# Kernel optimization log

Hardware: AMD Instinct MI355X
Metric: run time of the kernel (lower is better)

The kernel has to match this reference:

```python
import jax, jax.numpy as jnp
import numpy as np

N = 100000   # nodes
E = 1600000  # edges (avg degree 16)
F_IN, F_HID, F_OUT = 128, 128, 64


def _glorot_like(key, shape, fan_in):
    s = 1.0 / np.sqrt(fan_in)
    return jax.random.uniform(key, shape, jnp.float32, -s, s)


def setup_inputs():
    key = jax.random.key(0)
    ks = jax.random.split(key, 10)
    x = jax.random.normal(ks[0], (N, F_IN), jnp.float32)
    edge_index = jax.random.randint(ks[1], (2, E), 0, N, dtype=jnp.int64)
    # layer 0: GCNConv(128->128) + Linear(128->128)
    W0 = _glorot_like(ks[2], (F_IN, F_HID), F_IN)
    b0 = jnp.zeros((F_HID,), jnp.float32)
    Wl0 = _glorot_like(ks[3], (F_IN, F_HID), F_IN)
    bl0 = _glorot_like(ks[4], (F_HID,), F_IN)
    # layer 1: GCNConv(128->64) + Linear(128->64)
    W1 = _glorot_like(ks[5], (F_HID, F_OUT), F_HID)
    b1 = jnp.zeros((F_OUT,), jnp.float32)
    Wl1 = _glorot_like(ks[6], (F_HID, F_OUT), F_HID)
    bl1 = _glorot_like(ks[7], (F_OUT,), F_HID)
    return {"x": x, "edge_index": edge_index, "W0": W0, "b0": b0,
            "Wl0": Wl0, "bl0": bl0, "W1": W1, "b1": b1,
            "Wl1": Wl1, "bl1": bl1}


def _gcn_conv(x, W, b, src, dst, n):
    # PyG GCNConv: out = D^{-1/2} (A + I) D^{-1/2} (x W) + b
    h = x @ W                                      # [n, f_out]
    deg = jnp.ones((n,), x.dtype).at[dst].add(1.0)  # in-degree incl. self-loop
    dinv = jax.lax.rsqrt(deg)                      # [n]
    coef = dinv[src] * dinv[dst]                   # [E] edge norm
    agg = jax.ops.segment_sum(h[src] * coef[:, None], dst, num_segments=n)
    agg = agg + h * (dinv * dinv)[:, None]         # self-loop contribution
    return agg + b


def reference(x, edge_index, W0, b0, Wl0, bl0, W1, b1, Wl1, bl1):
    n = x.shape[0]
    src, dst = edge_index[0], edge_index[1]
    # layer 0 (inductive): conv(x) + lin(x), relu; dropout is identity in eval
    h = jax.nn.relu(_gcn_conv(x, W0, b0, src, dst, n) + x @ Wl0 + bl0)
    # output layer
    return _gcn_conv(h, W1, b1, src, dst, n) + h @ Wl1 + bl1
```

## Files before the change

### kernel.cpp

```cpp
#include <hip/hip_runtime.h>
#include <hip/hip_bf16.h>

#define NN 100000
#define EE 1600000
#define FF 128
#define FO 64

#define NR 256
#define RSZ 391
#define BCAP 8192
#define SE 5000
#define SBLK 320
#define GBLK0 782

typedef unsigned int u32;
typedef unsigned short u16;
typedef short s16x8 __attribute__((ext_vector_type(8)));
typedef float f32x4 __attribute__((ext_vector_type(4)));

__device__ __forceinline__ float bf_lo(u32 v) { return __uint_as_float(v << 16); }
__device__ __forceinline__ float bf_hi(u32 v) { return __uint_as_float(v & 0xffff0000u); }
__device__ __forceinline__ u16 f2bf(float f) {
    __hip_bfloat16 h = __float2bfloat16(f);
    return *(u16*)&h;
}
__device__ __forceinline__ u32 pk2(float a, float b) {
    return (u32)f2bf(a) | ((u32)f2bf(b) << 16);
}

__device__ __forceinline__ int ld_dst(const u32* w, int e, int f) {
    return f ? (int)w[2u * (u32)(EE + e)] : (int)w[(u32)(EE + e)];
}
__device__ __forceinline__ int ld_src(const u32* w, int e, int f) {
    return f ? (int)w[2u * (u32)e] : (int)w[(u32)e];
}

__device__ __forceinline__ int wave_iscan(int v, int lane) {
#pragma unroll
    for (int off = 1; off < 64; off <<= 1) {
        int t = __shfl_up(v, off);
        if (lane >= off) v += t;
    }
    return v;
}

__global__ __launch_bounds__(256) void k_prep(
    const float* __restrict__ W0, const float* __restrict__ Wl0,
    const float* __restrict__ b0, const float* __restrict__ bl0,
    const float* __restrict__ W1, const float* __restrict__ Wl1,
    const float* __restrict__ b1, const float* __restrict__ bl1,
    uint4* __restrict__ pb0, uint4* __restrict__ pb1,
    float* __restrict__ bb0, float* __restrict__ bb1) {
    const int t = threadIdx.x;
    if (blockIdx.x == 0 && t < FF) bb0[t] = b0[t] + bl0[t];
    if (blockIdx.x == 1 && t < FO) bb1[t] = b1[t] + bl1[t];
    int slot = blockIdx.x * 256 + t;
    if (slot < 4096) {
        int lane = slot & 63, nt = (slot >> 6) & 15, kb = slot >> 10;
        int c = 16 * nt + (lane & 15);
        int k0 = 32 * kb + 8 * (lane >> 4);
        u32 u[4];
#pragma unroll
        for (int p = 0; p < 4; ++p) {
            int ka = k0 + 2 * p, kb2 = k0 + 2 * p + 1;
            float v0 = (c < FF) ? W0[(size_t)ka * FF + c] : Wl0[(size_t)ka * FF + c - FF];
            float v1 = (c < FF) ? W0[(size_t)kb2 * FF + c] : Wl0[(size_t)kb2 * FF + c - FF];
            u[p] = pk2(v0, v1);
        }
        pb0[slot] = make_uint4(u[0], u[1], u[2], u[3]);
    } else if (slot < 6144) {
        int s = slot - 4096;
        int lane = s & 63, nt = (s >> 6) & 7, kb = s >> 9;
        int c = 16 * nt + (lane & 15);
        int q = 4 * kb + (lane >> 4);
        u32 u[4];
#pragma unroll
        for (int p = 0; p < 4; ++p) {
            int ra = 16 * (2 * p) + q;
            int rb = 16 * (2 * p + 1) + q;
            float v0 = (c < FO) ? W1[(size_t)ra * FO + c] : Wl1[(size_t)ra * FO + c - FO];
            float v1 = (c < FO) ? W1[(size_t)rb * FO + c] : Wl1[(size_t)rb * FO + c - FO];
            u[p] = pk2(v0, v1);
        }
        pb1[s] = make_uint4(u[0], u[1], u[2], u[3]);
    }
}

union SMem {
    struct {
        u16 inv[SE]; unsigned char rng[SE];
        int hist[NR], excl[NR], cur[NR], gbase[NR]; int wsum[8]; u32 fl;
    } sc;
    uint4 aLDS[128 * 16];
};

__device__ void role_gemm0(int bid, const float* __restrict__ x,
                           const uint4* __restrict__ pb0,
                           const float* __restrict__ bb0,
                           uint2* __restrict__ h0f8, uint4* __restrict__ linb4,
                           SMem& sm) {
    const int tid = threadIdx.x;
    const int n0 = bid * 128;
    {
        int r = tid >> 2, q = tid & 3;
        int node = n0 + r;
        uint4 ov[4];
        if (node < NN) {
            const float* src = &x[(size_t)node * FF + 32 * q];
#pragma unroll
            for (int i = 0; i < 4; ++i) {
                float4 f0 = *(const float4*)(src + 8 * i);
                float4 f1 = *(const float4*)(src + 8 * i + 4);
                ov[i] = make_uint4(pk2(f0.x, f0.y), pk2(f0.z, f0.w),
                                   pk2(f1.x, f1.y), pk2(f1.z, f1.w));
            }
        } else {
#pragma unroll
            for (int i = 0; i < 4; ++i) ov[i] = make_uint4(0, 0, 0, 0);
        }
#pragma unroll
        for (int i = 0; i < 4; ++i) {
            int chunk = 4 * q + i;
            sm.aLDS[r * 16 + (chunk ^ (r & 7))] = ov[i];
        }
    }
    __syncthreads();
    const int w = tid >> 6, l = tid & 63;
    const int lrow = l & 15, lhi = l >> 4;
    const int arow = 16 * w + lrow;
    f32x4 acc[16] = {};
#pragma unroll
    for (int kb = 0; kb < 4; ++kb) {
        int chunk = 4 * kb + lhi;
        uint4 av = sm.aLDS[arow * 16 + (chunk ^ (arow & 7))];
        s16x8 a = __builtin_bit_cast(s16x8, av);
#pragma unroll
        for (int nt = 0; nt < 16; ++nt) {
            uint4 bv = pb0[(kb * 16 + nt) * 64 + l];
            s16x8 b = __builtin_bit_cast(s16x8, bv);
            acc[nt] = __builtin_amdgcn_mfma_f32_16x16x32_bf16(a, b, acc[nt], 0, 0, 0);
        }
    }
#pragma unroll
    for (int j = 0; j < 4; ++j) {
        int node = n0 + 16 * w + 4 * lhi + j;
        u32 w0 = (u32)__builtin_amdgcn_cvt_pk_fp8_f32(acc[0][j], acc[1][j], 0, false);
        w0 = (u32)__builtin_amdgcn_cvt_pk_fp8_f32(acc[2][j], acc[3][j], (int)w0, true);
        u32 w1 = (u32)__builtin_amdgcn_cvt_pk_fp8_f32(acc[4][j], acc[5][j], 0, false);
        w1 = (u32)__builtin_amdgcn_cvt_pk_fp8_f32(acc[6][j], acc[7][j], (int)w1, true);
        h0f8[(size_t)node * 16 + lrow] = make_uint2(w0, w1);
        if (node >= NN) continue;
        uint4 lb;
        lb.x = pk2(acc[8][j] + bb0[lrow],       acc[9][j] + bb0[16 + lrow]);
        lb.y = pk2(acc[10][j] + bb0[32 + lrow], acc[11][j] + bb0[48 + lrow]);
        lb.z = pk2(acc[12][j] + bb0[64 + lrow], acc[13][j] + bb0[80 + lrow]);
        lb.w = pk2(acc[14][j] + bb0[96 + lrow], acc[15][j] + bb0[112 + lrow]);
        linb4[(size_t)node * 16 + lrow] = lb;
    }
}

__device__ void role_scatter(int sbid, const void* __restrict__ ei,
                             int* __restrict__ gCur, uint2* __restrict__ pairB,
                             SMem& sm) {
    const int tid = threadIdx.x;
    const int lane = tid & 63, wid = tid >> 6;
    const u32* w = (const u32*)ei;
    const int e0 = sbid * SE;
    if (tid == 0) sm.sc.fl = 0;
    if (tid < NR) { sm.sc.hist[tid] = 0; sm.sc.cur[tid] = 0; }
    __syncthreads();
    {
        u32 acc = 0;
#pragma unroll
        for (int r = 0; r < 4; ++r) acc |= w[2u * (u32)(e0 + tid + 512 * r) + 1];
        if (acc) atomicOr(&sm.sc.fl, 1u);
    }
    __syncthreads();
    const int f = (sm.sc.fl == 0) ? 1 : 0;
    for (int i = tid; i < SE; i += 512) {
        int dv = ld_dst(w, e0 + i, f);
        u32 r = (u32)dv / RSZ;
        sm.sc.rng[i] = (unsigned char)r;
        atomicAdd(&sm.sc.hist[r], 1);
    }
    __syncthreads();
    int v = (tid < NR) ? sm.sc.hist[tid] : 0;
    v = wave_iscan(v, lane);
    if (lane == 63) sm.sc.wsum[wid] = v;
    __syncthreads();
    if (tid < NR) {
        int add = 0;
#pragma unroll
        for (int k = 0; k < 3; ++k)
            if (k < wid) add += sm.sc.wsum[k];
        int incl = v + add;
        sm.sc.excl[tid] = incl - sm.sc.hist[tid];
        int r2 = (tid + sbid) & (NR - 1);
        sm.sc.gbase[r2] = atomicAdd(&gCur[r2], sm.sc.hist[r2]);
    }
    __syncthreads();
    for (int i = tid; i < SE; i += 512) {
        int r = sm.sc.rng[i];
        int p = atomicAdd(&sm.sc.cur[r], 1);
        sm.sc.inv[sm.sc.excl[r] + p] = (u16)i;
    }
    __syncthreads();
    for (int s = tid; s < SE; s += 512) {
        int i = sm.sc.inv[s];
        int r = sm.sc.rng[i];
        int dv = ld_dst(w, e0 + i, f);
        int sv = ld_src(w, e0 + i, f);
        int g = sm.sc.gbase[r] + (s - sm.sc.excl[r]);
        if (g < BCAP)
            pairB[(size_t)r * BCAP + g] = make_uint2((u32)dv, (u32)sv);
    }
}

__global__ __launch_bounds__(512) void k_mega(
    const float* __restrict__ x, const void* __restrict__ ei,
    int* __restrict__ gCur, uint2* __restrict__ pairB,
    const uint4* __restrict__ pb0, const float* __restrict__ bb0,
    uint2* __restrict__ h0f8, uint4* __restrict__ linb4) {
    __shared__ SMem sm;
    const int bid = blockIdx.x;
    if (bid < SBLK) {
        role_scatter(bid, ei, gCur, pairB, sm);
    } else {
        role_gemm0(bid - SBLK, x, pb0, bb0, h0f8, linb4, sm);
    }
}

__global__ __launch_bounds__(512) void k_fillrange(const uint2* __restrict__ pairB,
                                                   const int* __restrict__ gCur,
                                                   int* __restrict__ rp,
                                                   float* __restrict__ dinv,
                                                   int* __restrict__ col) {
    __shared__ int colbuf[BCAP];
    __shared__ int hist[RSZ], scn[RSZ], cur[RSZ];
    __shared__ int rb[NR];
    __shared__ int wsum[8];
    const int r = blockIdx.x;
    const int tid = threadIdx.x;
    const int lane = tid & 63, wid = tid >> 6;
    {
        int v = (tid < NR) ? gCur[tid] : 0;
        v = wave_iscan(v, lane);
        if (lane == 63) wsum[wid] = v;
        __syncthreads();
        if (tid < NR) {
            int add = 0;
#pragma unroll
            for (int k = 0; k < 3; ++k)
                if (k < wid) add += wsum[k];
            rb[tid] = v + add;
        }
        __syncthreads();
    }
    const int base = (r == 0) ? 0 : rb[r - 1];
    if (r == 0 && tid == 0) rp[NN] = rb[NR - 1];
    const int n = min(gCur[r], BCAP);
    const uint2* pb = &pairB[(size_t)r * BCAP];
    const int v0 = r * RSZ;
    for (int i = tid; i < RSZ; i += 512) { hist[i] = 0; cur[i] = 0; }
    __syncthreads();
    for (int j = tid; j < n; j += 512) atomicAdd(&hist[(int)pb[j].x - v0], 1);
    __syncthreads();
    {
        int v = (tid < RSZ) ? hist[tid] : 0;
        v = wave_iscan(v, lane);
        if (lane == 63) wsum[wid] = v;
        __syncthreads();
        int add = 0;
#pragma unroll
        for (int k = 0; k < 7; ++k)
            if (k < wid) add += wsum[k];
        if (tid < RSZ) scn[tid] = v + add;
    }
    if (tid < RSZ) {
        int v = v0 + tid;
        if (v < NN) {
            rp[v] = base + scn[tid] - hist[tid];
            dinv[v] = rsqrtf((float)hist[tid] + 1.0f);
        }
    }
    __syncthreads();
    for (int j = tid; j < n; j += 512) {
        uint2 pr = pb[j];
        int li = (int)pr.x - v0;
        int p = atomicAdd(&cur[li], 1);
        colbuf[scn[li] - hist[li] + p] = (int)pr.y;
    }
    __syncthreads();
    for (int j = tid; j < n; j += 512) col[base + j] = colbuf[j];
}

__global__ __launch_bounds__(256) void k_agg0(
    const int* __restrict__ rp, const int* __restrict__ col,
    const float* __restrict__ dinv, const uint2* __restrict__ h0f8,
    const uint4* __restrict__ linb4, uint4* __restrict__ hb) {
    const int i = blockIdx.x * 4 + (threadIdx.x >> 6);
    if (i >= NN) return;
    const int l = threadIdx.x & 63;
    const int q = l >> 4;
    const int c = l & 15;
    const int e0 = rp[i];
    const int cnt = rp[i + 1] - e0;
    const int cntv = cnt + 1;
    int j0;
    float dvL;
    if (l < cnt) {
        j0 = col[e0 + l];
        dvL = dinv[j0];
    } else if (l == cnt) {
        j0 = i;
        dvL = dinv[i];
    } else {
        j0 = NN;
        dvL = 0.f;
    }
    int offL = j0 << 7;
    const u32 oc = 8u * (u32)c;
    const char* hb8 = (const char*)h0f8;
    float a0 = 0.f, a1 = 0.f, a2 = 0.f, a3 = 0.f;
    float a4 = 0.f, a5 = 0.f, a6 = 0.f, a7 = 0.f;
#define ACC_FP8(vv, dd)                                                      \
    {                                                                        \
        auto d0 = __builtin_amdgcn_cvt_pk_f32_fp8((vv).x, false);            \
        auto d1 = __builtin_amdgcn_cvt_pk_f32_fp8((vv).x, true);             \
        auto d2 = __builtin_amdgcn_cvt_pk_f32_fp8((vv).y, false);            \
        auto d3 = __builtin_amdgcn_cvt_pk_f32_fp8((vv).y, true);             \
        a0 = fmaf(dd, d0[0], a0); a1 = fmaf(dd, d0[1], a1);                  \
        a2 = fmaf(dd, d1[0], a2); a3 = fmaf(dd, d1[1], a3);                  \
        a4 = fmaf(dd, d2[0], a4); a5 = fmaf(dd, d2[1], a5);                  \
        a6 = fmaf(dd, d3[0], a6); a7 = fmaf(dd, d3[1], a7);                  \
    }
    const int T = (min(cntv, 64) + 3) >> 2;
    int k = 0;
    for (; k + 4 <= T; k += 4) {
        int s = q + 4 * k;
        int oA = __shfl(offL, s);
        int oB = __shfl(offL, s + 4);
        int oC = __shfl(offL, s + 8);
        int oD = __shfl(offL, s + 12);
        float dA = __shfl(dvL, s);
        float dB = __shfl(dvL, s + 4);
        float dC = __shfl(dvL, s + 8);
        float dD = __shfl(dvL, s + 12);
        uint2 vA = *(const uint2*)(hb8 + ((u32)oA + oc));
        uint2 vB = *(const uint2*)(hb8 + ((u32)oB + oc));
        uint2 vC = *(const uint2*)(hb8 + ((u32)oC + oc));
        uint2 vD = *(const uint2*)(hb8 + ((u32)oD + oc));
        ACC_FP8(vA, dA);
        ACC_FP8(vB, dB);
        ACC_FP8(vC, dC);
        ACC_FP8(vD, dD);
    }
    for (; k < T; ++k) {
        int s = q + 4 * k;
        int o = __shfl(offL, s);
        float d = __shfl(dvL, s);
        uint2 v = *(const uint2*)(hb8 + ((u32)o + oc));
        ACC_FP8(v, d);
    }
    for (int e = 64 + q; e < cntv; e += 4) {
        int j = (e < cnt) ? col[e0 + e] : i;
        float d = dinv[j];
        uint2 v = *(const uint2*)(hb8 + ((u32)(j << 7) + oc));
        ACC_FP8(v, d);
    }
#undef ACC_FP8
#pragma unroll
    for (int off = 16; off < 64; off <<= 1) {
        a0 += __shfl_xor(a0, off);
        a1 += __shfl_xor(a1, off);
        a2 += __shfl_xor(a2, off);
        a3 += __shfl_xor(a3, off);
        a4 += __shfl_xor(a4, off);
        a5 += __shfl_xor(a5, off);
        a6 += __shfl_xor(a6, off);
        a7 += __shfl_xor(a7, off);
    }
    if (q == 0) {
        float di = dinv[i];
        uint4 lb = linb4[(size_t)i * 16 + c];
        uint4 ov;
        ov.x = pk2(fmaxf(fmaf(di, a0, bf_lo(lb.x)), 0.f),
                   fmaxf(fmaf(di, a1, bf_hi(lb.x)), 0.f));
        ov.y = pk2(fmaxf(fmaf(di, a2, bf_lo(lb.y)), 0.f),
                   fmaxf(fmaf(di, a3, bf_hi(lb.y)), 0.f));
        ov.z = pk2(fmaxf(fmaf(di, a4, bf_lo(lb.z)), 0.f),
                   fmaxf(fmaf(di, a5, bf_hi(lb.z)), 0.f));
        ov.w = pk2(fmaxf(fmaf(di, a6, bf_lo(lb.w)), 0.f),
                   fmaxf(fmaf(di, a7, bf_hi(lb.w)), 0.f));
        hb[(size_t)i * 16 + c] = ov;
    }
}

__global__ __launch_bounds__(256) void k_gemm1(
    const u16* __restrict__ h, const uint4* __restrict__ pb1,
    const float* __restrict__ bb1, const float* __restrict__ dinv,
    u16* __restrict__ h1s, float* __restrict__ out) {
    __shared__ uint4 aLDS[64 * 16];
    const int tid = threadIdx.x;
    const int n0 = blockIdx.x * 64;
    {
        int r = tid >> 2, q = tid & 3;
        int node = n0 + r;
        uint4 ov[4];
        if (node < NN) {
            const uint4* src = (const uint4*)&h[(size_t)node * FF + 32 * q];
#pragma unroll
            for (int i = 0; i < 4; ++i) ov[i] = src[i];
        } else {
#pragma unroll
            for (int i = 0; i < 4; ++i) ov[i] = make_uint4(0, 0, 0, 0);
        }
#pragma unroll
        for (int i = 0; i < 4; ++i) {
            int chunk = 4 * q + i;
            aLDS[r * 16 + (chunk ^ (r & 7))] = ov[i];
        }
    }
    __syncthreads();
    const int w = tid >> 6, l = tid & 63;
    const int lrow = l & 15, lhi = l >> 4;
    const int arow = 16 * w + lrow;
    f32x4 acc[8] = {};
#pragma unroll
    for (int kb = 0; kb < 4; ++kb) {
        int chunk = 4 * kb + lhi;
        uint4 av = aLDS[arow * 16 + (chunk ^ (arow & 7))];
        s16x8 a = __builtin_bit_cast(s16x8, av);
#pragma unroll
        for (int nt = 0; nt < 8; ++nt) {
            uint4 bv = pb1[(kb * 8 + nt) * 64 + l];
            s16x8 b = __builtin_bit_cast(s16x8, bv);
            acc[nt] = __builtin_amdgcn_mfma_f32_16x16x32_bf16(a, b, acc[nt], 0, 0, 0);
        }
    }
#pragma unroll
    for (int j = 0; j < 4; ++j) {
        int node = n0 + 16 * w + 4 * lhi + j;
        if (node >= NN) {
#pragma unroll
            for (int nt = 0; nt < 4; ++nt)
                h1s[(size_t)node * FO + 16 * nt + lrow] = 0;
            continue;
        }
        float di = dinv[node], d2 = di * di;
#pragma unroll
        for (int nt = 0; nt < 4; ++nt) {
            int c = 16 * nt + lrow;
            float hv = acc[nt][j];
            float lv = acc[nt + 4][j];
            h1s[(size_t)node * FO + c] = f2bf(di * hv);
            out[(size_t)node * FO + c] = fmaf(hv, d2, lv + bb1[c]);
        }
    }
}

__global__ __launch_bounds__(256) void k_agg1(
    const int* __restrict__ rp, const int* __restrict__ col,
    const float* __restrict__ dinv, const uint4* __restrict__ h1s,
    float* __restrict__ out) {
    const int i = blockIdx.x * 4 + (threadIdx.x >> 6);
    if (i >= NN) return;
    const int l = threadIdx.x & 63;
    const int g = l >> 3;
    const int c = l & 7;
    const int e0 = rp[i];
    const int cnt = rp[i + 1] - e0;
    int j0 = (l < cnt) ? col[e0 + l] : NN;
    int offL = j0 << 7;
    const u32 oc = 16u * (u32)c;
    const char* hs8 = (const char*)h1s;
    float a0 = 0.f, a1 = 0.f, a2 = 0.f, a3 = 0.f;
    float a4 = 0.f, a5 = 0.f, a6 = 0.f, a7 = 0.f;
    const int T = (min(cnt, 64) + 7) >> 3;
    int k = 0;
    for (; k + 2 <= T; k += 2) {
        int s = g + 8 * k;
        int oA = __shfl(offL, s);
        int oB = __shfl(offL, s + 8);
        uint4 vA = *(const uint4*)(hs8 + ((u32)oA + oc));
        uint4 vB = *(const uint4*)(hs8 + ((u32)oB + oc));
        a0 += bf_lo(vA.x) + bf_lo(vB.x);
        a1 += bf_hi(vA.x) + bf_hi(vB.x);
        a2 += bf_lo(vA.y) + bf_lo(vB.y);
        a3 += bf_hi(vA.y) + bf_hi(vB.y);
        a4 += bf_lo(vA.z) + bf_lo(vB.z);
        a5 += bf_hi(vA.z) + bf_hi(vB.z);
        a6 += bf_lo(vA.w) + bf_lo(vB.w);
        a7 += bf_hi(vA.w) + bf_hi(vB.w);
    }
    for (; k < T; ++k) {
        int s = g + 8 * k;
        int o = __shfl(offL, s);
        uint4 v = *(const uint4*)(hs8 + ((u32)o + oc));
        a0 += bf_lo(v.x); a1 += bf_hi(v.x); a2 += bf_lo(v.y); a3 += bf_hi(v.y);
        a4 += bf_lo(v.z); a5 += bf_hi(v.z); a6 += bf_lo(v.w); a7 += bf_hi(v.w);
    }
    for (int e = 64 + g; e < cnt; e += 8) {
        int j = col[e0 + e];
        uint4 v = *(const uint4*)(hs8 + ((u32)(j << 7) + oc));
        a0 += bf_lo(v.x); a1 += bf_hi(v.x); a2 += bf_lo(v.y); a3 += bf_hi(v.y);
        a4 += bf_lo(v.z); a5 += bf_hi(v.z); a6 += bf_lo(v.w); a7 += bf_hi(v.w);
    }
#pragma unroll
    for (int off = 8; off < 64; off <<= 1) {
        a0 += __shfl_xor(a0, off);
        a1 += __shfl_xor(a1, off);
        a2 += __shfl_xor(a2, off);
        a3 += __shfl_xor(a3, off);
        a4 += __shfl_xor(a4, off);
        a5 += __shfl_xor(a5, off);
        a6 += __shfl_xor(a6, off);
        a7 += __shfl_xor(a7, off);
    }
    if (g == 0) {
        float di = dinv[i];
        size_t o = (size_t)i * FO + 8 * c;
        float4 c0 = *(const float4*)&out[o];
        float4 c1 = *(const float4*)&out[o + 4];
        c0.x = fmaf(di, a0, c0.x);
        c0.y = fmaf(di, a1, c0.y);
        c0.z = fmaf(di, a2, c0.z);
        c0.w = fmaf(di, a3, c0.w);
        c1.x = fmaf(di, a4, c1.x);
        c1.y = fmaf(di, a5, c1.y);
        c1.z = fmaf(di, a6, c1.z);
        c1.w = fmaf(di, a7, c1.w);
        *(float4*)&out[o] = c0;
        *(float4*)&out[o + 4] = c1;
    }
}

extern "C" void kernel_launch(void* const* d_in, const int* in_sizes, int n_in,
                              void* d_out, int out_size, void* d_ws, size_t ws_size,
                              hipStream_t stream) {
    const float* x   = (const float*)d_in[0];
    const void*  ei  = d_in[1];
    const float* W0  = (const float*)d_in[2];
    const float* b0  = (const float*)d_in[3];
    const float* Wl0 = (const float*)d_in[4];
    const float* bl0 = (const float*)d_in[5];
    const float* W1  = (const float*)d_in[6];
    const float* b1  = (const float*)d_in[7];
    const float* Wl1 = (const float*)d_in[8];
    const float* bl1 = (const float*)d_in[9];
    float* out = (float*)d_out;

    char* p = (char*)d_ws;
    auto alloc = [&](size_t bytes) -> void* {
        void* r = (void*)p;
        p += (bytes + 255) & ~(size_t)255;
        return r;
    };
    int*   gCur   = (int*)alloc(NR * 4);
    int*   rp     = (int*)alloc((size_t)(NN + 1) * 4);
    int*   col    = (int*)alloc((size_t)EE * 4);
    uint2* pairB  = (uint2*)alloc((size_t)NR * BCAP * 8);
    float* dinv   = (float*)alloc((size_t)NN * 4);
    uint4* pb0    = (uint4*)alloc(4096 * 16);
    uint4* pb1    = (uint4*)alloc(2048 * 16);
    float* bb0    = (float*)alloc(FF * 4);
    float* bb1    = (float*)alloc(FO * 4);
    uint2* h0f8   = (uint2*)alloc((size_t)(NN + 128) * FF);
    uint4* linb4  = (uint4*)alloc((size_t)NN * FF * 2);
    u16*   h1s    = (u16*)alloc((size_t)(NN + 64) * FO * 2);
    u16*   hb     = (u16*)alloc((size_t)NN * FF * 2);

    hipMemsetAsync(gCur, 0, NR * 4, stream);
    k_prep<<<24, 256, 0, stream>>>(W0, Wl0, b0, bl0, W1, Wl1, b1, bl1,
                                   pb0, pb1, bb0, bb1);
    k_mega<<<GBLK0 + SBLK, 512, 0, stream>>>(x, ei, gCur, pairB, pb0, bb0,
                                             h0f8, linb4);
    k_fillrange<<<NR, 512, 0, stream>>>(pairB, gCur, rp, dinv, col);
    k_agg0<<<(NN + 3) / 4, 256, 0, stream>>>(rp, col, dinv, h0f8, linb4,
                                             (uint4*)hb);
    k_gemm1<<<(NN + 63) / 64, 256, 0, stream>>>(hb, pb1, bb1, dinv, h1s, out);
    k_agg1<<<(NN + 3) / 4, 256, 0, stream>>>(rp, col, dinv, (const uint4*)h1s, out);
}
```

Baseline: 174.3 us.

## Process four nodes per wave in aggregation and simplify scatter/fillrange staging

Both aggregation kernels now assign four consecutive nodes to each wavefront, prefetching all four row ranges and neighbor indices up front so their loads overlap. The grid shrinks accordingly. The scatter pass drops its local sort-by-range staging and writes pairs directly using per-range atomic cursors. Fillrange writes col entries straight to global memory instead of staging them in shared memory. These cut launch overhead, shared-memory work and barriers, at the cost of less coalesced global writes and more registers per thread.

```diff
diff --git a/kernel.cpp b/kernel.cpp
--- a/kernel.cpp
+++ b/kernel.cpp
@@ -12,6 +12,8 @@
 #define SE 5000
 #define SBLK 320
 #define GBLK0 782
+#define NPW 4
+#define AGG_GRID 6250
 
 typedef unsigned int u32;
 typedef unsigned short u16;
@@ -88,8 +90,7 @@
 
 union SMem {
     struct {
-        u16 inv[SE]; unsigned char rng[SE];
-        int hist[NR], excl[NR], cur[NR], gbase[NR]; int wsum[8]; u32 fl;
+        int hist[NR], cur[NR], gbase[NR]; u32 fl;
     } sc;
     uint4 aLDS[128 * 16];
 };
@@ -163,7 +164,6 @@
                              int* __restrict__ gCur, uint2* __restrict__ pairB,
                              SMem& sm) {
     const int tid = threadIdx.x;
-    const int lane = tid & 63, wid = tid >> 6;
     const u32* w = (const u32*)ei;
     const int e0 = sbid * SE;
     if (tid == 0) sm.sc.fl = 0;
@@ -179,38 +179,20 @@
     const int f = (sm.sc.fl == 0) ? 1 : 0;
     for (int i = tid; i < SE; i += 512) {
         int dv = ld_dst(w, e0 + i, f);
-        u32 r = (u32)dv / RSZ;
-        sm.sc.rng[i] = (unsigned char)r;
-        atomicAdd(&sm.sc.hist[r], 1);
-    }
-    __syncthreads();
-    int v = (tid < NR) ? sm.sc.hist[tid] : 0;
-    v = wave_iscan(v, lane);
-    if (lane == 63) sm.sc.wsum[wid] = v;
+        atomicAdd(&sm.sc.hist[(u32)dv / RSZ], 1);
+    }
     __syncthreads();
     if (tid < NR) {
-        int add = 0;
-#pragma unroll
-        for (int k = 0; k < 3; ++k)
-            if (k < wid) add += sm.sc.wsum[k];
-        int incl = v + add;
-        sm.sc.excl[tid] = incl - sm.sc.hist[tid];
         int r2 = (tid + sbid) & (NR - 1);
         sm.sc.gbase[r2] = atomicAdd(&gCur[r2], sm.sc.hist[r2]);
     }
     __syncthreads();
     for (int i = tid; i < SE; i += 512) {
-        int r = sm.sc.rng[i];
-        int p = atomicAdd(&sm.sc.cur[r], 1);
-        sm.sc.inv[sm.sc.excl[r] + p] = (u16)i;
-    }
-    __syncthreads();
-    for (int s = tid; s < SE; s += 512) {
-        int i = sm.sc.inv[s];
-        int r = sm.sc.rng[i];
         int dv = ld_dst(w, e0 + i, f);
         int sv = ld_src(w, e0 + i, f);
-        int g = sm.sc.gbase[r] + (s - sm.sc.excl[r]);
+        u32 r = (u32)dv / RSZ;
+        int p = atomicAdd(&sm.sc.cur[r], 1);
+        int g = sm.sc.gbase[r] + p;
         if (g < BCAP)
             pairB[(size_t)r * BCAP + g] = make_uint2((u32)dv, (u32)sv);
     }
@@ -235,7 +217,6 @@
                                                    int* __restrict__ rp,
                                                    float* __restrict__ dinv,
                                                    int* __restrict__ col) {
-    __shared__ int colbuf[BCAP];
     __shared__ int hist[RSZ], scn[RSZ], cur[RSZ];
     __shared__ int rb[NR];
     __shared__ int wsum[8];
@@ -288,41 +269,38 @@
         uint2 pr = pb[j];
         int li = (int)pr.x - v0;
         int p = atomicAdd(&cur[li], 1);
-        colbuf[scn[li] - hist[li] + p] = (int)pr.y;
-    }
-    __syncthreads();
-    for (int j = tid; j < n; j += 512) col[base + j] = colbuf[j];
+        col[base + scn[li] - hist[li] + p] = (int)pr.y;
+    }
 }
 
 __global__ __launch_bounds__(256) void k_agg0(
     const int* __restrict__ rp, const int* __restrict__ col,
     const float* __restrict__ dinv, const uint2* __restrict__ h0f8,
     const uint4* __restrict__ linb4, uint4* __restrict__ hb) {
-    const int i = blockIdx.x * 4 + (threadIdx.x >> 6);
-    if (i >= NN) return;
+    const int wv = blockIdx.x * 4 + (threadIdx.x >> 6);
+    const int i0 = wv * NPW;
+    if (i0 >= NN) return;
     const int l = threadIdx.x & 63;
     const int q = l >> 4;
     const int c = l & 15;
-    const int e0 = rp[i];
-    const int cnt = rp[i + 1] - e0;
-    const int cntv = cnt + 1;
-    int j0;
-    float dvL;
-    if (l < cnt) {
-        j0 = col[e0 + l];
-        dvL = dinv[j0];
-    } else if (l == cnt) {
-        j0 = i;
-        dvL = dinv[i];
-    } else {
-        j0 = NN;
-        dvL = 0.f;
-    }
-    int offL = j0 << 7;
+    int rpv = (l <= NPW) ? rp[i0 + l] : 0;
+    int rpk[NPW + 1];
+#pragma unroll
+    for (int k = 0; k <= NPW; ++k) rpk[k] = __shfl(rpv, k);
+    int offL[NPW];
+    float dvL[NPW];
+#pragma unroll
+    for (int k = 0; k < NPW; ++k) {
+        int cntk = rpk[k + 1] - rpk[k];
+        int jj;
+        if (l < cntk) jj = col[rpk[k] + l];
+        else if (l == cntk) jj = i0 + k;
+        else jj = NN;
+        dvL[k] = (jj < NN) ? dinv[jj] : 0.f;
+        offL[k] = jj << 7;
+    }
     const u32 oc = 8u * (u32)c;
     const char* hb8 = (const char*)h0f8;
-    float a0 = 0.f, a1 = 0.f, a2 = 0.f, a3 = 0.f;
-    float a4 = 0.f, a5 = 0.f, a6 = 0.f, a7 = 0.f;
 #define ACC_FP8(vv, dd)                                                      \
     {                                                                        \
         auto d0 = __builtin_amdgcn_cvt_pk_f32_fp8((vv).x, false);            \
@@ -334,66 +312,75 @@
         a4 = fmaf(dd, d2[0], a4); a5 = fmaf(dd, d2[1], a5);                  \
         a6 = fmaf(dd, d3[0], a6); a7 = fmaf(dd, d3[1], a7);                  \
     }
-    const int T = (min(cntv, 64) + 3) >> 2;
-    int k = 0;
-    for (; k + 4 <= T; k += 4) {
-        int s = q + 4 * k;
-        int oA = __shfl(offL, s);
-        int oB = __shfl(offL, s + 4);
-        int oC = __shfl(offL, s + 8);
-        int oD = __shfl(offL, s + 12);
-        float dA = __shfl(dvL, s);
-        float dB = __shfl(dvL, s + 4);
-        float dC = __shfl(dvL, s + 8);
-        float dD = __shfl(dvL, s + 12);
-        uint2 vA = *(const uint2*)(hb8 + ((u32)oA + oc));
-        uint2 vB = *(const uint2*)(hb8 + ((u32)oB + oc));
-        uint2 vC = *(const uint2*)(hb8 + ((u32)oC + oc));
-        uint2 vD = *(const uint2*)(hb8 + ((u32)oD + oc));
-        ACC_FP8(vA, dA);
-        ACC_FP8(vB, dB);
-        ACC_FP8(vC, dC);
-        ACC_FP8(vD, dD);
-    }
-    for (; k < T; ++k) {
-        int s = q + 4 * k;
-        int o = __shfl(offL, s);
-        float d = __shfl(dvL, s);
-        uint2 v = *(const uint2*)(hb8 + ((u32)o + oc));
-        ACC_FP8(v, d);
-    }
-    for (int e = 64 + q; e < cntv; e += 4) {
-        int j = (e < cnt) ? col[e0 + e] : i;
-        float d = dinv[j];
-        uint2 v = *(const uint2*)(hb8 + ((u32)(j << 7) + oc));
-        ACC_FP8(v, d);
+#pragma unroll
+    for (int k = 0; k < NPW; ++k) {
+        const int i = i0 + k;
+        const int cnt = rpk[k + 1] - rpk[k];
+        const int cntv = cnt + 1;
+        float a0 = 0.f, a1 = 0.f, a2 = 0.f, a3 = 0.f;
+        float a4 = 0.f, a5 = 0.f, a6 = 0.f, a7 = 0.f;
+        const int T = (min(cntv, 64) + 3) >> 2;
+        int t = 0;
+        for (; t + 4 <= T; t += 4) {
+            int s = q + 4 * t;
+            int oA = __shfl(offL[k], s);
+            int oB = __shfl(offL[k], s + 4);
+            int oC = __shfl(offL[k], s + 8);
+            int oD = __shfl(offL[k], s + 12);
+            float dA = __shfl(dvL[k], s);
+            float dB = __shfl(dvL[k], s + 4);
+            float dC = __shfl(dvL[k], s + 8);
+            float dD = __shfl(dvL[k], s + 12);
+            uint2 vA = *(const uint2*)(hb8 + ((u32)oA + oc));
+            uint2 vB = *(const uint2*)(hb8 + ((u32)oB + oc));
+            uint2 vC = *(const uint2*)(hb8 + ((u32)oC + oc));
+            uint2 vD = *(const uint2*)(hb8 + ((u32)oD + oc));
+            ACC_FP8(vA, dA);
+            ACC_FP8(vB, dB);
+            ACC_FP8(vC, dC);
+            ACC_FP8(vD, dD);
+        }
+        for (; t < T; ++t) {
+            int s = q + 4 * t;
+            int o = __shfl(offL[k], s);
+            float d = __shfl(dvL[k], s);
+            uint2 v = *(const uint2*)(hb8 + ((u32)o + oc));
+            ACC_FP8(v, d);
+        }
+        for (int e = 64 + q; e < cntv; e += 4) {
+            int j = (e < cnt) ? col[rpk[k] + e] : i;
+            float d = dinv[j];
+            uint2 v = *(const uint2*)(hb8 + ((u32)(j << 7) + oc));
+            ACC_FP8(v, d);
+        }
+#pragma unroll
+        for (int off = 16; off < 64; off <<= 1) {
+            a0 += __shfl_xor(a0, off);
+            a1 += __shfl_xor(a1, off);
+            a2 += __shfl_xor(a2, off);
+            a3 += __shfl_xor(a3, off);
+            a4 += __shfl_xor(a4, off);
+            a5 += __shfl_xor(a5, off);
+            a6 += __shfl_xor(a6, off);
+            a7 += __shfl_xor(a7, off);
+        }
+        float di = __shfl(dvL[k], min(cnt, 63));
+        if (cnt > 63) di = dinv[i];
+        if (q == 0) {
+            uint4 lb = linb4[(size_t)i * 16 + c];
+            uint4 ov;
+            ov.x = pk2(fmaxf(fmaf(di, a0, bf_lo(lb.x)), 0.f),
+                       fmaxf(fmaf(di, a1, bf_hi(lb.x)), 0.f));
+            ov.y = pk2(fmaxf(fmaf(di, a2, bf_lo(lb.y)), 0.f),
+                       fmaxf(fmaf(di, a3, bf_hi(lb.y)), 0.f));
+            ov.z = pk2(fmaxf(fmaf(di, a4, bf_lo(lb.z)), 0.f),
+                       fmaxf(fmaf(di, a5, bf_hi(lb.z)), 0.f));
+            ov.w = pk2(fmaxf(fmaf(di, a6, bf_lo(lb.w)), 0.f),
+                       fmaxf(fmaf(di, a7, bf_hi(lb.w)), 0.f));
+            hb[(size_t)i * 16 + c] = ov;
+        }
     }
 #undef ACC_FP8
-#pragma unroll
-    for (int off = 16; off < 64; off <<= 1) {
-        a0 += __shfl_xor(a0, off);
-        a1 += __shfl_xor(a1, off);
-        a2 += __shfl_xor(a2, off);
-        a3 += __shfl_xor(a3, off);
-        a4 += __shfl_xor(a4, off);
-        a5 += __shfl_xor(a5, off);
-        a6 += __shfl_xor(a6, off);
-        a7 += __shfl_xor(a7, off);
-    }
-    if (q == 0) {
-        float di = dinv[i];
-        uint4 lb = linb4[(size_t)i * 16 + c];
-        uint4 ov;
-        ov.x = pk2(fmaxf(fmaf(di, a0, bf_lo(lb.x)), 0.f),
-                   fmaxf(fmaf(di, a1, bf_hi(lb.x)), 0.f));
-        ov.y = pk2(fmaxf(fmaf(di, a2, bf_lo(lb.y)), 0.f),
-                   fmaxf(fmaf(di, a3, bf_hi(lb.y)), 0.f));
-        ov.z = pk2(fmaxf(fmaf(di, a4, bf_lo(lb.z)), 0.f),
-                   fmaxf(fmaf(di, a5, bf_hi(lb.z)), 0.f));
-        ov.w = pk2(fmaxf(fmaf(di, a6, bf_lo(lb.w)), 0.f),
-                   fmaxf(fmaf(di, a7, bf_hi(lb.w)), 0.f));
-        hb[(size_t)i * 16 + c] = ov;
-    }
 }
 
 __global__ __launch_bounds__(256) void k_gemm1(
@@ -463,75 +450,88 @@
     const int* __restrict__ rp, const int* __restrict__ col,
     const float* __restrict__ dinv, const uint4* __restrict__ h1s,
     float* __restrict__ out) {
-    const int i = blockIdx.x * 4 + (threadIdx.x >> 6);
-    if (i >= NN) return;
+    const int wv = blockIdx.x * 4 + (threadIdx.x >> 6);
+    const int i0 = wv * NPW;
+    if (i0 >= NN) return;
     const int l = threadIdx.x & 63;
     const int g = l >> 3;
     const int c = l & 7;
-    const int e0 = rp[i];
-    const int cnt = rp[i + 1] - e0;
-    int j0 = (l < cnt) ? col[e0 + l] : NN;
-    int offL = j0 << 7;
+    int rpv = (l <= NPW) ? rp[i0 + l] : 0;
+    int rpk[NPW + 1];
+#pragma unroll
+    for (int k = 0; k <= NPW; ++k) rpk[k] = __shfl(rpv, k);
+    int offL[NPW];
+#pragma unroll
+    for (int k = 0; k < NPW; ++k) {
+        int cntk = rpk[k + 1] - rpk[k];
+        int jj = (l < cntk) ? col[rpk[k] + l] : NN;
+        offL[k] = jj << 7;
+    }
     const u32 oc = 16u * (u32)c;
     const char* hs8 = (const char*)h1s;
-    float a0 = 0.f, a1 = 0.f, a2 = 0.f, a3 = 0.f;
-    float a4 = 0.f, a5 = 0.f, a6 = 0.f, a7 = 0.f;
-    const int T = (min(cnt, 64) + 7) >> 3;
-    int k = 0;
-    for (; k + 2 <= T; k += 2) {
-        int s = g + 8 * k;
-        int oA = __shfl(offL, s);
-        int oB = __shfl(offL, s + 8);
-        uint4 vA = *(const uint4*)(hs8 + ((u32)oA + oc));
-        uint4 vB = *(const uint4*)(hs8 + ((u32)oB + oc));
-        a0 += bf_lo(vA.x) + bf_lo(vB.x);
-        a1 += bf_hi(vA.x) + bf_hi(vB.x);
-        a2 += bf_lo(vA.y) + bf_lo(vB.y);
-        a3 += bf_hi(vA.y) + bf_hi(vB.y);
-        a4 += bf_lo(vA.z) + bf_lo(vB.z);
-        a5 += bf_hi(vA.z) + bf_hi(vB.z);
-        a6 += bf_lo(vA.w) + bf_lo(vB.w);
-        a7 += bf_hi(vA.w) + bf_hi(vB.w);
-    }
-    for (; k < T; ++k) {
-        int s = g + 8 * k;
-        int o = __shfl(offL, s);
-        uint4 v = *(const uint4*)(hs8 + ((u32)o + oc));
-        a0 += bf_lo(v.x); a1 += bf_hi(v.x); a2 += bf_lo(v.y); a3 += bf_hi(v.y);
-        a4 += bf_lo(v.z); a5 += bf_hi(v.z); a6 += bf_lo(v.w); a7 += bf_hi(v.w);
-    }
-    for (int e = 64 + g; e < cnt; e += 8) {
-        int j = col[e0 + e];
-        uint4 v = *(const uint4*)(hs8 + ((u32)(j << 7) + oc));
-        a0 += bf_lo(v.x); a1 += bf_hi(v.x); a2 += bf_lo(v.y); a3 += bf_hi(v.y);
-        a4 += bf_lo(v.z); a5 += bf_hi(v.z); a6 += bf_lo(v.w); a7 += bf_hi(v.w);
-    }
-#pragma unroll
-    for (int off = 8; off < 64; off <<= 1) {
-        a0 += __shfl_xor(a0, off);
-        a1 += __shfl_xor(a1, off);
-        a2 += __shfl_xor(a2, off);
-        a3 += __shfl_xor(a3, off);
-        a4 += __shfl_xor(a4, off);
-        a5 += __shfl_xor(a5, off);
-        a6 += __shfl_xor(a6, off);
-        a7 += __shfl_xor(a7, off);
-    }
-    if (g == 0) {
-        float di = dinv[i];
-        size_t o = (size_t)i * FO + 8 * c;
-        float4 c0 = *(const float4*)&out[o];
-        float4 c1 = *(const float4*)&out[o + 4];
-        c0.x = fmaf(di, a0, c0.x);
-        c0.y = fmaf(di, a1, c0.y);
-        c0.z = fmaf(di, a2, c0.z);
-        c0.w = fmaf(di, a3, c0.w);
-        c1.x = fmaf(di, a4, c1.x);
-        c1.y = fmaf(di, a5, c1.y);
-        c1.z = fmaf(di, a6, c1.z);
-        c1.w = fmaf(di, a7, c1.w);
-        *(float4*)&out[o] = c0;
-        *(float4*)&out[o + 4] = c1;
+#pragma unroll
+    for (int k = 0; k < NPW; ++k) {
+        const int i = i0 + k;
+        const int cnt = rpk[k + 1] - rpk[k];
+        float a0 = 0.f, a1 = 0.f, a2 = 0.f, a3 = 0.f;
+        float a4 = 0.f, a5 = 0.f, a6 = 0.f, a7 = 0.f;
+        const int T = (min(cnt, 64) + 7) >> 3;
+        int t = 0;
+        for (; t + 2 <= T; t += 2) {
+            int s = g + 8 * t;
+            int oA = __shfl(offL[k], s);
+            int oB = __shfl(offL[k], s + 8);
+            uint4 vA = *(const uint4*)(hs8 + ((u32)oA + oc));
+            uint4 vB = *(const uint4*)(hs8 + ((u32)oB + oc));
+            a0 += bf_lo(vA.x) + bf_lo(vB.x);
+            a1 += bf_hi(vA.x) + bf_hi(vB.x);
+            a2 += bf_lo(vA.y) + bf_lo(vB.y);
+            a3 += bf_hi(vA.y) + bf_hi(vB.y);
+            a4 += bf_lo(vA.z) + bf_lo(vB.z);
+            a5 += bf_hi(vA.z) + bf_hi(vB.z);
+            a6 += bf_lo(vA.w) + bf_lo(vB.w);
+            a7 += bf_hi(vA.w) + bf_hi(vB.w);
+        }
+        for (; t < T; ++t) {
+            int s = g + 8 * t;
+            int o = __shfl(offL[k], s);
+            uint4 v = *(const uint4*)(hs8 + ((u32)o + oc));
+            a0 += bf_lo(v.x); a1 += bf_hi(v.x); a2 += bf_lo(v.y); a3 += bf_hi(v.y);
+            a4 += bf_lo(v.z); a5 += bf_hi(v.z); a6 += bf_lo(v.w); a7 += bf_hi(v.w);
+        }
+        for (int e = 64 + g; e < cnt; e += 8) {
+            int j = col[rpk[k] + e];
+            uint4 v = *(const uint4*)(hs8 + ((u32)(j << 7) + oc));
+            a0 += bf_lo(v.x); a1 += bf_hi(v.x); a2 += bf_lo(v.y); a3 += bf_hi(v.y);
+            a4 += bf_lo(v.z); a5 += bf_hi(v.z); a6 += bf_lo(v.w); a7 += bf_hi(v.w);
+        }
+#pragma unroll
+        for (int off = 8; off < 64; off <<= 1) {
+            a0 += __shfl_xor(a0, off);
+            a1 += __shfl_xor(a1, off);
+            a2 += __shfl_xor(a2, off);
+            a3 += __shfl_xor(a3, off);
+            a4 += __shfl_xor(a4, off);
+            a5 += __shfl_xor(a5, off);
+            a6 += __shfl_xor(a6, off);
+            a7 += __shfl_xor(a7, off);
+        }
+        if (g == 0) {
+            float di = dinv[i];
+            size_t o = (size_t)i * FO + 8 * c;
+            float4 c0 = *(const float4*)&out[o];
+            float4 c1 = *(const float4*)&out[o + 4];
+            c0.x = fmaf(di, a0, c0.x);
+            c0.y = fmaf(di, a1, c0.y);
+            c0.z = fmaf(di, a2, c0.z);
+            c0.w = fmaf(di, a3, c0.w);
+            c1.x = fmaf(di, a4, c1.x);
+            c1.y = fmaf(di, a5, c1.y);
+            c1.z = fmaf(di, a6, c1.z);
+            c1.w = fmaf(di, a7, c1.w);
+            *(float4*)&out[o] = c0;
+            *(float4*)&out[o + 4] = c1;
+        }
     }
 }
 
@@ -576,8 +576,8 @@
     k_mega<<<GBLK0 + SBLK, 512, 0, stream>>>(x, ei, gCur, pairB, pb0, bb0,
                                              h0f8, linb4);
     k_fillrange<<<NR, 512, 0, stream>>>(pairB, gCur, rp, dinv, col);
-    k_agg0<<<(NN + 3) / 4, 256, 0, stream>>>(rp, col, dinv, h0f8, linb4,
-                                             (uint4*)hb);
+    k_agg0<<<AGG_GRID, 256, 0, stream>>>(rp, col, dinv, h0f8, linb4,
+                                         (uint4*)hb);
     k_gemm1<<<(NN + 63) / 64, 256, 0, stream>>>(hb, pb1, bb1, dinv, h1s, out);
-    k_agg1<<<(NN + 3) / 4, 256, 0, stream>>>(rp, col, dinv, (const uint4*)h1s, out);
-}
+    k_agg1<<<AGG_GRID, 256, 0, stream>>>(rp, col, dinv, (const uint4*)h1s, out);
+}
```

Result: slower. 180.6 us (+3.6%).

## Retile layer-0 GEMM waves to 32 rows by 8 column tiles; scatter col directly

Applied to the files above, without the earlier changes.

The layer-0 GEMM role now assigns each wave 32 rows and half the output column tiles, rather than 16 rows and all 16 tiles. Each B fragment load from global memory then feeds two MFMAs, halving B traffic per MFMA and the accumulators per thread, at the cost of twice as many A reads from LDS. Separately, k_fillrange drops its LDS staging buffer and writes column indices straight to global memory. That frees shared memory and removes a barrier, but the global writes become scattered instead of coalesced.

```diff
diff --git a/kernel.cpp b/kernel.cpp
--- a/kernel.cpp
+++ b/kernel.cpp
@@ -127,35 +127,48 @@
     __syncthreads();
     const int w = tid >> 6, l = tid & 63;
     const int lrow = l & 15, lhi = l >> 4;
-    const int arow = 16 * w + lrow;
-    f32x4 acc[16] = {};
+    const int wrow = w & 3;
+    const int half = w >> 2;
+    f32x4 acc[2][8] = {};
 #pragma unroll
     for (int kb = 0; kb < 4; ++kb) {
-        int chunk = 4 * kb + lhi;
-        uint4 av = sm.aLDS[arow * 16 + (chunk ^ (arow & 7))];
-        s16x8 a = __builtin_bit_cast(s16x8, av);
-#pragma unroll
-        for (int nt = 0; nt < 16; ++nt) {
+        s16x8 a[2];
+#pragma unroll
+        for (int rt = 0; rt < 2; ++rt) {
+            int arow = 32 * wrow + 16 * rt + lrow;
+            int chunk = 4 * kb + lhi;
+            uint4 av = sm.aLDS[arow * 16 + (chunk ^ (arow & 7))];
+            a[rt] = __builtin_bit_cast(s16x8, av);
+        }
+#pragma unroll
+        for (int nt8 = 0; nt8 < 8; ++nt8) {
+            int nt = 8 * half + nt8;
             uint4 bv = pb0[(kb * 16 + nt) * 64 + l];
             s16x8 b = __builtin_bit_cast(s16x8, bv);
-            acc[nt] = __builtin_amdgcn_mfma_f32_16x16x32_bf16(a, b, acc[nt], 0, 0, 0);
-        }
-    }
-#pragma unroll
-    for (int j = 0; j < 4; ++j) {
-        int node = n0 + 16 * w + 4 * lhi + j;
-        u32 w0 = (u32)__builtin_amdgcn_cvt_pk_fp8_f32(acc[0][j], acc[1][j], 0, false);
-        w0 = (u32)__builtin_amdgcn_cvt_pk_fp8_f32(acc[2][j], acc[3][j], (int)w0, true);
-        u32 w1 = (u32)__builtin_amdgcn_cvt_pk_fp8_f32(acc[4][j], acc[5][j], 0, false);
-        w1 = (u32)__builtin_amdgcn_cvt_pk_fp8_f32(acc[6][j], acc[7][j], (int)w1, true);
-        h0f8[(size_t)node * 16 + lrow] = make_uint2(w0, w1);
-        if (node >= NN) continue;
-        uint4 lb;
-        lb.x = pk2(acc[8][j] + bb0[lrow],       acc[9][j] + bb0[16 + lrow]);
-        lb.y = pk2(acc[10][j] + bb0[32 + lrow], acc[11][j] + bb0[48 + lrow]);
-        lb.z = pk2(acc[12][j] + bb0[64 + lrow], acc[13][j] + bb0[80 + lrow]);
-        lb.w = pk2(acc[14][j] + bb0[96 + lrow], acc[15][j] + bb0[112 + lrow]);
-        linb4[(size_t)node * 16 + lrow] = lb;
+            acc[0][nt8] = __builtin_amdgcn_mfma_f32_16x16x32_bf16(a[0], b, acc[0][nt8], 0, 0, 0);
+            acc[1][nt8] = __builtin_amdgcn_mfma_f32_16x16x32_bf16(a[1], b, acc[1][nt8], 0, 0, 0);
+        }
+    }
+#pragma unroll
+    for (int rt = 0; rt < 2; ++rt) {
+#pragma unroll
+        for (int j = 0; j < 4; ++j) {
+            int node = n0 + 32 * wrow + 16 * rt + 4 * lhi + j;
+            if (half == 0) {
+                u32 w0 = (u32)__builtin_amdgcn_cvt_pk_fp8_f32(acc[rt][0][j], acc[rt][1][j], 0, false);
+                w0 = (u32)__builtin_amdgcn_cvt_pk_fp8_f32(acc[rt][2][j], acc[rt][3][j], (int)w0, true);
+                u32 w1 = (u32)__builtin_amdgcn_cvt_pk_fp8_f32(acc[rt][4][j], acc[rt][5][j], 0, false);
+                w1 = (u32)__builtin_amdgcn_cvt_pk_fp8_f32(acc[rt][6][j], acc[rt][7][j], (int)w1, true);
+                h0f8[(size_t)node * 16 + lrow] = make_uint2(w0, w1);
+            } else if (node < NN) {
+                uint4 lb;
+                lb.x = pk2(acc[rt][0][j] + bb0[lrow],      acc[rt][1][j] + bb0[16 + lrow]);
+                lb.y = pk2(acc[rt][2][j] + bb0[32 + lrow], acc[rt][3][j] + bb0[48 + lrow]);
+                lb.z = pk2(acc[rt][4][j] + bb0[64 + lrow], acc[rt][5][j] + bb0[80 + lrow]);
+                lb.w = pk2(acc[rt][6][j] + bb0[96 + lrow], acc[rt][7][j] + bb0[112 + lrow]);
+                linb4[(size_t)node * 16 + lrow] = lb;
+            }
+        }
     }
 }
 
@@ -235,7 +248,6 @@
                                                    int* __restrict__ rp,
                                                    float* __restrict__ dinv,
                                                    int* __restrict__ col) {
-    __shared__ int colbuf[BCAP];
     __shared__ int hist[RSZ], scn[RSZ], cur[RSZ];
     __shared__ int rb[NR];
     __shared__ int wsum[8];
@@ -288,10 +300,8 @@
         uint2 pr = pb[j];
         int li = (int)pr.x - v0;
         int p = atomicAdd(&cur[li], 1);
-        colbuf[scn[li] - hist[li] + p] = (int)pr.y;
-    }
-    __syncthreads();
-    for (int j = tid; j < n; j += 512) col[base + j] = colbuf[j];
+        col[base + scn[li] - hist[li] + p] = (int)pr.y;
+    }
 }
 
 __global__ __launch_bounds__(256) void k_agg0(
```

Result: no change. 174.5 us (+0.1%).
